# Kernel tuning notes

Hardware: AMD Instinct MI355X
Metric: run time of the kernel (lower is better)

## Reference

```python
import jax, jax.numpy as jnp
import numpy as np

KH = KW = 3
PAD = 1
STRIDE = 1
C_IN = 32
C_OUT = 16
H = W = 64
B = 64
H_OUT = (H - KH + 2 * PAD) // STRIDE + 1
W_OUT = (W - KW + 2 * PAD) // STRIDE + 1
S = H_OUT * W_OUT
K = C_IN * KH * KW


def unfold_2d(x):
    # x: [B, C, H, W] -> [B, C*KH*KW, S], torch.nn.functional.unfold ordering
    xp = jnp.pad(x, ((0, 0), (0, 0), (PAD, PAD), (PAD, PAD)))
    patches = []
    for i in range(KH):
        for j in range(KW):
            patches.append(xp[:, :, i:i + H_OUT * STRIDE:STRIDE, j:j + W_OUT * STRIDE:STRIDE])
    u = jnp.stack(patches, axis=2)  # [B, C, KH*KW, H_OUT, W_OUT]
    return u.reshape(x.shape[0], K, S)


def setup_inputs() -> dict:
    key = jax.random.key(0)
    k1, k2, k3 = jax.random.split(key, 3)
    X = jax.random.normal(k1, (B, C_IN, H, W), dtype=jnp.float32)
    # kaiming normal (linear): std = 1/sqrt(fan_in), fan_in = K for each location's GEMM
    weight = jax.random.normal(k2, (S, K, C_OUT), dtype=jnp.float32) / jnp.sqrt(jnp.float32(K))
    # xavier uniform over [H_OUT, W_OUT]
    lim = np.sqrt(6.0 / (H_OUT + W_OUT))
    bias = jax.random.uniform(k3, (H_OUT, W_OUT), dtype=jnp.float32, minval=-lim, maxval=lim)
    return {"X": X, "weight": weight, "bias": bias}


def reference(X, weight, bias):
    ufld = unfold_2d(X)                               # [B, K, S]
    ufld = ufld + bias.reshape(1, 1, -1)              # bias added per-location to patches
    h = jnp.einsum('bks,skc->bcs', ufld, weight)      # per-location unshared GEMM
    return h.reshape(X.shape[0], C_OUT, H_OUT, W_OUT)
```

## Files before the change

kernel.cpp:

```cpp
#include <hip/hip_runtime.h>
#include <stdint.h>
#include <stddef.h>

#define HOUT 64
#define WOUT 64
#define CIN  32
#define COUT 16
#define BATCH 64
#define SLOC 4096
#define KTOT 288
#define HPAD 66

typedef __attribute__((ext_vector_type(8))) short  short8;
typedef __attribute__((ext_vector_type(4))) float  floatx4;

static __device__ __forceinline__ unsigned short f2bf(float f) {
    union { float f; unsigned int u; } v; v.f = f;
    unsigned int u = v.u;
    unsigned int r = (u + 0x7FFFu + ((u >> 16) & 1u)) >> 16;
    return (unsigned short)r;
}

__global__ __launch_bounds__(256) void zero_border_kernel(unsigned short* __restrict__ xt) {
    int bid = blockIdx.x;
    int h1, w1;
    if (bid < 66)       { h1 = 0;  w1 = bid; }
    else if (bid < 132) { h1 = 65; w1 = bid - 66; }
    else { int r = bid - 132; h1 = (r >> 1) + 1; w1 = (r & 1) ? 65 : 0; }
    uint4* dst = (uint4*)(xt + (size_t)(h1 * HPAD + w1) * 2048);
    dst[threadIdx.x] = uint4{0u, 0u, 0u, 0u};
}

__global__ __launch_bounds__(256) void transpose_kernel(const float* __restrict__ X,
                                                        unsigned short* __restrict__ xt) {
    int h = blockIdx.x;
    int b = blockIdx.y;
    int t = threadIdx.x;
    int w  = t >> 2;
    int cg = t & 3;

    const float* xb = X + (((size_t)b * CIN + cg * 8) * HOUT + h) * WOUT + w;
    unsigned short v[8];
#pragma unroll
    for (int j = 0; j < 8; ++j)
        v[j] = f2bf(xb[(size_t)j * HOUT * WOUT]);

    uint4 pack;
    pack.x = (unsigned)v[0] | ((unsigned)v[1] << 16);
    pack.y = (unsigned)v[2] | ((unsigned)v[3] << 16);
    pack.z = (unsigned)v[4] | ((unsigned)v[5] << 16);
    pack.w = (unsigned)v[6] | ((unsigned)v[7] << 16);

    *(uint4*)(xt + (size_t)((h + 1) * HPAD + (w + 1)) * 2048 + b * CIN + cg * 8) = pack;
}

__global__ __launch_bounds__(256) void varconv_kernel(const unsigned short* __restrict__ xt,
                                                      const float* __restrict__ Wg,
                                                      const float* __restrict__ bias,
                                                      float* __restrict__ out) {
    __shared__ float lds[16 * 16 * 32];

    int id = blockIdx.x;
    int g  = ((id >> 4) << 3) | (id & 7);
    int hh = (id >> 3) & 1;
    int s0 = g * 16;
    int y  = s0 >> 6;
    int x0 = s0 & 63;
    int B0 = hh * 32;

    int lane = threadIdx.x & 63, wv = threadIdx.x >> 6;
    int q = lane >> 4;
    int n = lane & 15;

#pragma unroll
    for (int i = 0; i < 4; ++i) {
        int sl = wv * 4 + i;
        int s  = s0 + sl;
        int x  = x0 + sl;

        const float* wb = Wg + (size_t)s * (KTOT * COUT) + (size_t)(8 * q) * 9 * COUT + n;
        short8 bf[9];
        float csum = 0.f;
#pragma unroll
        for (int t = 0; t < 9; ++t) {
            float w8[8];
#pragma unroll
            for (int j = 0; j < 8; ++j)
                w8[j] = wb[(size_t)(j * 9 + t) * COUT];
#pragma unroll
            for (int j = 0; j < 8; ++j) {
                csum += w8[j];
                bf[t][j] = (short)f2bf(w8[j]);
            }
        }
        csum += __shfl_xor(csum, 16, 64);
        csum += __shfl_xor(csum, 32, 64);
        float badd = bias[s] * csum;

#pragma unroll
        for (int mt = 0; mt < 2; ++mt) {
            const unsigned short* ab = xt + (size_t)(B0 + mt * 16 + n) * CIN + q * 8;
            floatx4 acc = {0.f, 0.f, 0.f, 0.f};
#pragma unroll
            for (int t = 0; t < 9; ++t) {
                const int cy = t / 3, cx = t % 3;
                int pix = (y + cy) * HPAD + (x + cx);
                short8 af = *(const short8*)(ab + (size_t)pix * 2048);
                acc = __builtin_amdgcn_mfma_f32_16x16x32_bf16(af, bf[t], acc, 0, 0, 0);
            }
            int bcl   = mt * 4 + q;
            int chunk = bcl ^ (n & 7);
            floatx4 v = {acc[0] + badd, acc[1] + badd, acc[2] + badd, acc[3] + badd};
            *(floatx4*)&lds[n * 512 + sl * 32 + chunk * 4] = v;
        }
    }

    __syncthreads();

    int c   = lane >> 2;
    int slg = lane & 3;
#pragma unroll
    for (int it = 0; it < 2; ++it) {
        int bcl   = wv + 4 * it;
        int chunk = bcl ^ (c & 7);
        floatx4 vj[4];
#pragma unroll
        for (int j = 0; j < 4; ++j) {
            int sl = slg * 4 + j;
            vj[j] = *(floatx4*)&lds[c * 512 + sl * 32 + chunk * 4];
        }
#pragma unroll
        for (int i2 = 0; i2 < 4; ++i2) {
            int b = B0 + bcl * 4 + i2;
            floatx4 o = {vj[0][i2], vj[1][i2], vj[2][i2], vj[3][i2]};
            *(floatx4*)(out + ((size_t)(b * COUT + c)) * SLOC + s0 + slg * 4) = o;
        }
    }
}

extern "C" void kernel_launch(void* const* d_in, const int* in_sizes, int n_in,
                              void* d_out, int out_size, void* d_ws, size_t ws_size,
                              hipStream_t stream) {
    const float* X    = (const float*)d_in[0];
    const float* Wg   = (const float*)d_in[1];
    const float* bias = (const float*)d_in[2];
    float* out = (float*)d_out;

    unsigned short* xt = (unsigned short*)d_ws;

    zero_border_kernel<<<260, 256, 0, stream>>>(xt);
    transpose_kernel<<<dim3(64, 64), 256, 0, stream>>>(X, xt);
    varconv_kernel<<<512, 256, 0, stream>>>(xt, Wg, bias, out);
}
```

Baseline: 176.3 us.

## Split varconv batch into four 16-wide quarters per block, doubling grid

Each block of the main kernel now handles 16 batch rows instead of 32, so the grid doubles to 1024 blocks, LDS use is halved and launch bounds request 4 blocks per CU. All weight loads are issued before the bf16 conversion to expose more memory-level parallelism. The aim is better occupancy and latency hiding, but every weight slice is now loaded and converted four times instead of twice, which adds global traffic on a large weight tensor.

Result: no change. 173.8 us (-1.4%).

```diff
diff --git a/kernel.cpp b/kernel.cpp
--- a/kernel.cpp
+++ b/kernel.cpp
@@ -54,19 +54,20 @@
     *(uint4*)(xt + (size_t)((h + 1) * HPAD + (w + 1)) * 2048 + b * CIN + cg * 8) = pack;
 }
 
-__global__ __launch_bounds__(256) void varconv_kernel(const unsigned short* __restrict__ xt,
-                                                      const float* __restrict__ Wg,
-                                                      const float* __restrict__ bias,
-                                                      float* __restrict__ out) {
-    __shared__ float lds[16 * 16 * 32];
+__global__ __launch_bounds__(256, 4) void varconv_kernel(const unsigned short* __restrict__ xt,
+                                                         const float* __restrict__ Wg,
+                                                         const float* __restrict__ bias,
+                                                         float* __restrict__ out) {
+    __shared__ float lds[16 * 16 * 16];
 
     int id = blockIdx.x;
-    int g  = ((id >> 4) << 3) | (id & 7);
-    int hh = (id >> 3) & 1;
+    int lo = id & 7;
+    int q4 = (id >> 3) & 3;
+    int g  = ((id >> 5) << 3) | lo;
     int s0 = g * 16;
     int y  = s0 >> 6;
     int x0 = s0 & 63;
-    int B0 = hh * 32;
+    int B0 = q4 * 16;
 
     int lane = threadIdx.x & 63, wv = threadIdx.x >> 6;
     int q = lane >> 4;
@@ -79,40 +80,38 @@
         int x  = x0 + sl;
 
         const float* wb = Wg + (size_t)s * (KTOT * COUT) + (size_t)(8 * q) * 9 * COUT + n;
-        short8 bf[9];
-        float csum = 0.f;
+        float w[9][8];
 #pragma unroll
-        for (int t = 0; t < 9; ++t) {
-            float w8[8];
+        for (int t = 0; t < 9; ++t)
 #pragma unroll
             for (int j = 0; j < 8; ++j)
-                w8[j] = wb[(size_t)(j * 9 + t) * COUT];
+                w[t][j] = wb[(size_t)(j * 9 + t) * COUT];
+
+        float csum = 0.f;
+        short8 bf[9];
+#pragma unroll
+        for (int t = 0; t < 9; ++t)
 #pragma unroll
             for (int j = 0; j < 8; ++j) {
-                csum += w8[j];
-                bf[t][j] = (short)f2bf(w8[j]);
+                csum += w[t][j];
+                bf[t][j] = (short)f2bf(w[t][j]);
             }
-        }
         csum += __shfl_xor(csum, 16, 64);
         csum += __shfl_xor(csum, 32, 64);
         float badd = bias[s] * csum;
 
+        const unsigned short* ab = xt + (size_t)(B0 + n) * CIN + q * 8;
+        floatx4 acc = {0.f, 0.f, 0.f, 0.f};
 #pragma unroll
-        for (int mt = 0; mt < 2; ++mt) {
-            const unsigned short* ab = xt + (size_t)(B0 + mt * 16 + n) * CIN + q * 8;
-            floatx4 acc = {0.f, 0.f, 0.f, 0.f};
-#pragma unroll
-            for (int t = 0; t < 9; ++t) {
-                const int cy = t / 3, cx = t % 3;
-                int pix = (y + cy) * HPAD + (x + cx);
-                short8 af = *(const short8*)(ab + (size_t)pix * 2048);
-                acc = __builtin_amdgcn_mfma_f32_16x16x32_bf16(af, bf[t], acc, 0, 0, 0);
-            }
-            int bcl   = mt * 4 + q;
-            int chunk = bcl ^ (n & 7);
-            floatx4 v = {acc[0] + badd, acc[1] + badd, acc[2] + badd, acc[3] + badd};
-            *(floatx4*)&lds[n * 512 + sl * 32 + chunk * 4] = v;
+        for (int t = 0; t < 9; ++t) {
+            const int cy = t / 3, cx = t % 3;
+            int pix = (y + cy) * HPAD + (x + cx);
+            short8 af = *(const short8*)(ab + (size_t)pix * 2048);
+            acc = __builtin_amdgcn_mfma_f32_16x16x32_bf16(af, bf[t], acc, 0, 0, 0);
         }
+        int slot = q ^ (n & 3);
+        floatx4 v = {acc[0] + badd, acc[1] + badd, acc[2] + badd, acc[3] + badd};
+        *(floatx4*)&lds[n * 256 + sl * 16 + slot * 4] = v;
     }
 
     __syncthreads();
@@ -120,21 +119,15 @@
     int c   = lane >> 2;
     int slg = lane & 3;
 #pragma unroll
-    for (int it = 0; it < 2; ++it) {
-        int bcl   = wv + 4 * it;
-        int chunk = bcl ^ (c & 7);
-        floatx4 vj[4];
+    for (int i2 = 0; i2 < 4; ++i2) {
+        int ib   = wv * 4 + i2;
+        int slot = (ib >> 2) ^ (c & 3);
+        float o0[4];
 #pragma unroll
-        for (int j = 0; j < 4; ++j) {
-            int sl = slg * 4 + j;
-            vj[j] = *(floatx4*)&lds[c * 512 + sl * 32 + chunk * 4];
-        }
-#pragma unroll
-        for (int i2 = 0; i2 < 4; ++i2) {
-            int b = B0 + bcl * 4 + i2;
-            floatx4 o = {vj[0][i2], vj[1][i2], vj[2][i2], vj[3][i2]};
-            *(floatx4*)(out + ((size_t)(b * COUT + c)) * SLOC + s0 + slg * 4) = o;
-        }
+        for (int e = 0; e < 4; ++e)
+            o0[e] = lds[c * 256 + (slg * 4 + e) * 16 + slot * 4 + (ib & 3)];
+        floatx4 o = {o0[0], o0[1], o0[2], o0[3]};
+        *(floatx4*)(out + ((size_t)((B0 + ib) * COUT + c)) * SLOC + s0 + slg * 4) = o;
     }
 }
 
@@ -150,5 +143,5 @@
 
     zero_border_kernel<<<260, 256, 0, stream>>>(xt);
     transpose_kernel<<<dim3(64, 64), 256, 0, stream>>>(X, xt);
-    varconv_kernel<<<512, 256, 0, stream>>>(xt, Wg, bias, out);
+    varconv_kernel<<<1024, 256, 0, stream>>>(xt, Wg, bias, out);
 }
```
